# Optimization experiments

Hardware: AMD Instinct MI355X
Metric: run time of the kernel (lower is better)

## Reference

```python
import jax, jax.numpy as jnp
import numpy as np

B, T, I, H, O = 2048, 512, 1, 64, 1


def setup_inputs() -> dict:
    key = jax.random.key(0)
    ks = jax.random.split(key, 7)
    k = 1.0 / np.sqrt(H)  # PyTorch default uniform init bound
    u = lambda kk, sh: jax.random.uniform(kk, sh, jnp.float32, -k, k)
    return {
        "x": jax.random.normal(ks[0], (B, T, I), jnp.float32),
        "w_ih": u(ks[1], (4 * H, I)),   # gate order: i, f, g, o (PyTorch)
        "w_hh": u(ks[2], (4 * H, H)),
        "b_ih": u(ks[3], (4 * H,)),
        "b_hh": u(ks[4], (4 * H,)),
        "w_lin": u(ks[5], (O, H)),
        "b_lin": u(ks[6], (O,)),
    }


def _lstm_last_h(x, w_ih, w_hh, b_ih, b_hh):
    """Single-layer LSTM (PyTorch gate order i,f,g,o), returns h at the last step."""
    Bsz = x.shape[0]
    Hs = w_hh.shape[1]
    # Precompute input contribution for all timesteps: [B, T, 4H]
    gx_all = jnp.einsum('bti,gi->btg', x, w_ih) + b_ih + b_hh

    def step(carry, gx):
        h, c = carry
        g = gx + h @ w_hh.T  # [B, 4H]
        i, f, gg, o = jnp.split(g, 4, axis=-1)
        i = jax.nn.sigmoid(i)
        f = jax.nn.sigmoid(f)
        gg = jnp.tanh(gg)
        o = jax.nn.sigmoid(o)
        c = f * c + i * gg
        h = o * jnp.tanh(c)
        return (h, c), None

    h0 = jnp.zeros((Bsz, Hs), x.dtype)
    (h_last, _), _ = jax.lax.scan(step, (h0, h0), jnp.swapaxes(gx_all, 0, 1))
    return h_last  # == out[:, -1, :]


def reference(x, w_ih, w_hh, b_ih, b_hh, w_lin, b_lin):
    h = _lstm_last_h(x, w_ih, w_hh, b_ih, b_hh)
    return h @ w_lin.T + b_lin  # [B, O]
```

## Files before the change

kernel.cpp:

```cpp
#include <hip/hip_runtime.h>


typedef float    f32x4 __attribute__((ext_vector_type(4)));
typedef _Float16 f16x8 __attribute__((ext_vector_type(8)));

namespace {
constexpr int Bsz = 2048;
constexpr int Tsz = 512;
constexpr int NBW = 2;
}

__device__ __forceinline__ float rcp_f(float v)  { return __builtin_amdgcn_rcpf(v); }
__device__ __forceinline__ float exp2_f(float v) { return __builtin_amdgcn_exp2f(v); }

__device__ __forceinline__ float sigm_s(float gs)  { return rcp_f(1.0f + exp2_f(gs)); }
__device__ __forceinline__ float tanh_s(float gs)  { return fmaf(2.0f, rcp_f(1.0f + exp2_f(gs)), -1.0f); }
__device__ __forceinline__ float tanh_plain(float v) {
    return fmaf(2.0f, rcp_f(1.0f + exp2_f(v * -2.88539008178f)), -1.0f);
}

__global__ __launch_bounds__(256, 4)
void lstm_v7(const float* __restrict__ x,
             const float* __restrict__ w_ih,
             const float* __restrict__ w_hh,
             const float* __restrict__ b_ih,
             const float* __restrict__ b_hh,
             const float* __restrict__ w_lin,
             const float* __restrict__ b_lin,
             float* __restrict__ out)
{
    __shared__ __align__(16) float x_lds[Tsz][NBW];
    __shared__ __align__(16) char  hA[16 * 128];
    __shared__ __align__(16) float g_raw[256 * NBW];
    __shared__ float part[2 * NBW];

    const int tid = threadIdx.x;
    const int wv  = tid >> 6;
    const int ln  = tid & 63;
    const int col = ln & 15;
    const int grp = ln >> 4;
    const int b0  = blockIdx.x * NBW;

    constexpr float LOG2E = 1.44269504089f;
    const float s = (wv == 2) ? (-2.0f * LOG2E) : (-LOG2E);

    {
        const int b  = tid >> 7;
        const int t4 = tid & 127;
        const float4 v = ((const float4*)(x + (size_t)(b0 + b) * Tsz))[t4];
        x_lds[t4 * 4 + 0][b] = v.x;
        x_lds[t4 * 4 + 1][b] = v.y;
        x_lds[t4 * 4 + 2][b] = v.z;
        x_lds[t4 * 4 + 3][b] = v.w;
    }

    f16x8 Wf[4][2];
    float wihc[4], biasc[4];
    #pragma unroll
    for (int tn = 0; tn < 4; ++tn) {
        const int gate = wv * 64 + tn * 16 + col;
        const float* wrow = w_hh + (size_t)gate * 64;
        #pragma unroll
        for (int kc = 0; kc < 2; ++kc) {
            f16x8 w;
            #pragma unroll
            for (int e = 0; e < 8; ++e)
                w[e] = (_Float16)(wrow[kc * 32 + grp * 8 + e] * s);
            Wf[tn][kc] = w;
        }
        wihc[tn]  = w_ih[gate] * s;
        biasc[tn] = (b_ih[gate] + b_hh[gate]) * s;
    }

    const int sw    = (col & 7) << 4;
    const int aoff0 = col * 128 + ((grp * 16) ^ sw);
    const int aoff1 = col * 128 + ((64 + grp * 16) ^ sw);

    const int pb = tid & 1;
    const int pj = (tid >> 1) & 63;
    const float wlin  = w_lin[pj];
    const int   hwoff = pb * 128 + ((2 * pj) ^ (pb << 4));

    ((float2*)hA)[tid] = make_float2(0.0f, 0.0f);

    float c = 0.0f, h = 0.0f;

    __syncthreads();

    for (int t = 0; t < Tsz; ++t) {
        const float2 xb = *(const float2*)&x_lds[t][0];
        const f16x8 A0 = *(const f16x8*)(hA + aoff0);
        const f16x8 A1 = *(const f16x8*)(hA + aoff1);

        f32x4 acc[4];
        #pragma unroll
        for (int tn = 0; tn < 4; ++tn) {
            acc[tn][0] = fmaf(xb.x, wihc[tn], biasc[tn]);
            acc[tn][1] = fmaf(xb.y, wihc[tn], biasc[tn]);
            acc[tn][2] = biasc[tn];
            acc[tn][3] = biasc[tn];
        }
        #pragma unroll
        for (int tn = 0; tn < 4; ++tn)
            acc[tn] = __builtin_amdgcn_mfma_f32_16x16x32_f16(A0, Wf[tn][0], acc[tn], 0, 0, 0);
        #pragma unroll
        for (int tn = 0; tn < 4; ++tn)
            acc[tn] = __builtin_amdgcn_mfma_f32_16x16x32_f16(A1, Wf[tn][1], acc[tn], 0, 0, 0);

        if (ln < 16) {
            #pragma unroll
            for (int tn = 0; tn < 4; ++tn) {
                float2 gw;
                gw.x = acc[tn][0];
                gw.y = acc[tn][1];
                *(float2*)&g_raw[(wv * 64 + tn * 16 + ln) * 2] = gw;
            }
        }
        __syncthreads();

        if (tid < 128) {
            const float gi = g_raw[tid +   0];
            const float gf = g_raw[tid + 128];
            const float gg = g_raw[tid + 256];
            const float go = g_raw[tid + 384];

            const float ig = sigm_s(gi);
            const float fg = sigm_s(gf);
            const float tg = tanh_s(gg);
            const float og = sigm_s(go);
            c = fmaf(fg, c, ig * tg);
            h = og * tanh_plain(c);

            *(_Float16*)(hA + hwoff) = (_Float16)h;
        }
        __syncthreads();
    }

    if (tid < 128) {
        float p = h * wlin;
        #pragma unroll
        for (int off = 2; off < 64; off <<= 1)
            p += __shfl_xor(p, off, 64);
        if (ln < 2) part[wv * 2 + ln] = p;
    }
    __syncthreads();
    if (tid < NBW)
        out[b0 + tid] = part[tid] + part[2 + tid] + b_lin[0];
}

extern "C" void kernel_launch(void* const* d_in, const int* in_sizes, int n_in,
                              void* d_out, int out_size, void* d_ws, size_t ws_size,
                              hipStream_t stream) {
    const float* x     = (const float*)d_in[0];
    const float* w_ih  = (const float*)d_in[1];
    const float* w_hh  = (const float*)d_in[2];
    const float* b_ih  = (const float*)d_in[3];
    const float* b_hh  = (const float*)d_in[4];
    const float* w_lin = (const float*)d_in[5];
    const float* b_lin = (const float*)d_in[6];
    float* out = (float*)d_out;

    dim3 grid(Bsz / NBW);
    dim3 block(256);
    lstm_v7<<<grid, block, 0, stream>>>(x, w_ih, w_hh, b_ih, b_hh,
                                        w_lin, b_lin, out);
}
```

Baseline: 347.4 us.

## Ping-pong two batch chains per block to overlap MFMA with activations

```diff
diff --git a/kernel.cpp b/kernel.cpp
--- a/kernel.cpp
+++ b/kernel.cpp
@@ -7,7 +7,7 @@
 namespace {
 constexpr int Bsz = 2048;
 constexpr int Tsz = 512;
-constexpr int NBW = 2;
+constexpr int NBW = 8;
 }
 
 __device__ __forceinline__ float rcp_f(float v)  { return __builtin_amdgcn_rcpf(v); }
@@ -19,8 +19,8 @@
     return fmaf(2.0f, rcp_f(1.0f + exp2_f(v * -2.88539008178f)), -1.0f);
 }
 
-__global__ __launch_bounds__(256, 4)
-void lstm_v7(const float* __restrict__ x,
+__global__ __launch_bounds__(512, 2)
+void lstm_v8(const float* __restrict__ x,
              const float* __restrict__ w_ih,
              const float* __restrict__ w_hh,
              const float* __restrict__ b_ih,
@@ -30,9 +30,9 @@
              float* __restrict__ out)
 {
     __shared__ __align__(16) float x_lds[Tsz][NBW];
-    __shared__ __align__(16) char  hA[16 * 128];
-    __shared__ __align__(16) float g_raw[256 * NBW];
-    __shared__ float part[2 * NBW];
+    __shared__ __align__(16) char  hA[2][16 * 128];
+    __shared__ __align__(16) float g_raw[2][256 * 4];
+    __shared__ float part[32];
 
     const int tid = threadIdx.x;
     const int wv  = tid >> 6;
@@ -42,11 +42,14 @@
     const int b0  = blockIdx.x * NBW;
 
     constexpr float LOG2E = 1.44269504089f;
-    const float s = (wv == 2) ? (-2.0f * LOG2E) : (-LOG2E);
+    const int   gtype = wv >> 1;
+    const float s     = (gtype == 2) ? (-2.0f * LOG2E) : (-LOG2E);
 
-    {
-        const int b  = tid >> 7;
-        const int t4 = tid & 127;
+    #pragma unroll
+    for (int it = 0; it < 2; ++it) {
+        const int i  = tid + it * 512;
+        const int b  = i >> 7;
+        const int t4 = i & 127;
         const float4 v = ((const float4*)(x + (size_t)(b0 + b) * Tsz))[t4];
         x_lds[t4 * 4 + 0][b] = v.x;
         x_lds[t4 * 4 + 1][b] = v.y;
@@ -54,11 +57,11 @@
         x_lds[t4 * 4 + 3][b] = v.w;
     }
 
-    f16x8 Wf[4][2];
-    float wihc[4], biasc[4];
+    f16x8 Wf[2][2];
+    float wihc[2], biasc[2];
     #pragma unroll
-    for (int tn = 0; tn < 4; ++tn) {
-        const int gate = wv * 64 + tn * 16 + col;
+    for (int tn = 0; tn < 2; ++tn) {
+        const int gate = wv * 32 + tn * 16 + col;
         const float* wrow = w_hh + (size_t)gate * 64;
         #pragma unroll
         for (int kc = 0; kc < 2; ++kc) {
@@ -76,8 +79,10 @@
     const int aoff0 = col * 128 + ((grp * 16) ^ sw);
     const int aoff1 = col * 128 + ((64 + grp * 16) ^ sw);
 
-    const int pb = tid & 1;
-    const int pj = (tid >> 1) & 63;
+    const int myChain = (wv >= 4) ? 0 : 1;
+    const int idx = tid & 255;
+    const int pb  = idx & 3;
+    const int pj  = idx >> 2;
     const float wlin  = w_lin[pj];
     const int   hwoff = pb * 128 + ((2 * pj) ^ (pb << 4));
 
@@ -85,67 +90,76 @@
 
     float c = 0.0f, h = 0.0f;
 
+#define MFMA_STEP(ch, tt)                                                      \
+    {                                                                          \
+        const float4 xb = *(const float4*)&x_lds[(tt)][(ch) * 4];              \
+        const f16x8 A0 = *(const f16x8*)(hA[(ch)] + aoff0);                    \
+        const f16x8 A1 = *(const f16x8*)(hA[(ch)] + aoff1);                    \
+        f32x4 a0, a1;                                                          \
+        a0[0] = fmaf(xb.x, wihc[0], biasc[0]);                                 \
+        a0[1] = fmaf(xb.y, wihc[0], biasc[0]);                                 \
+        a0[2] = fmaf(xb.z, wihc[0], biasc[0]);                                 \
+        a0[3] = fmaf(xb.w, wihc[0], biasc[0]);                                 \
+        a1[0] = fmaf(xb.x, wihc[1], biasc[1]);                                 \
+        a1[1] = fmaf(xb.y, wihc[1], biasc[1]);                                 \
+        a1[2] = fmaf(xb.z, wihc[1], biasc[1]);                                 \
+        a1[3] = fmaf(xb.w, wihc[1], biasc[1]);                                 \
+        a0 = __builtin_amdgcn_mfma_f32_16x16x32_f16(A0, Wf[0][0], a0, 0, 0, 0);\
+        a0 = __builtin_amdgcn_mfma_f32_16x16x32_f16(A1, Wf[0][1], a0, 0, 0, 0);\
+        a1 = __builtin_amdgcn_mfma_f32_16x16x32_f16(A0, Wf[1][0], a1, 0, 0, 0);\
+        a1 = __builtin_amdgcn_mfma_f32_16x16x32_f16(A1, Wf[1][1], a1, 0, 0, 0);\
+        if (ln < 16) {                                                         \
+            *(f32x4*)&g_raw[(ch)][(wv * 32 + ln) * 4]      = a0;               \
+            *(f32x4*)&g_raw[(ch)][(wv * 32 + 16 + ln) * 4] = a1;               \
+        }                                                                      \
+    }
+
+#define ACT_STEP(ch)                                                           \
+    if (myChain == (ch)) {                                                     \
+        const float gi = g_raw[(ch)][idx +   0];                               \
+        const float gf = g_raw[(ch)][idx + 256];                               \
+        const float gg = g_raw[(ch)][idx + 512];                               \
+        const float go = g_raw[(ch)][idx + 768];                               \
+        const float ig = sigm_s(gi);                                           \
+        const float fg = sigm_s(gf);                                           \
+        const float tg = tanh_s(gg);                                           \
+        const float og = sigm_s(go);                                           \
+        c = fmaf(fg, c, ig * tg);                                              \
+        h = og * tanh_plain(c);                                                \
+        *(_Float16*)(hA[(ch)] + hwoff) = (_Float16)h;                          \
+    }
+
     __syncthreads();
 
-    for (int t = 0; t < Tsz; ++t) {
-        const float2 xb = *(const float2*)&x_lds[t][0];
-        const f16x8 A0 = *(const f16x8*)(hA + aoff0);
-        const f16x8 A1 = *(const f16x8*)(hA + aoff1);
+    MFMA_STEP(0, 0)
+    __syncthreads();
 
-        f32x4 acc[4];
-        #pragma unroll
-        for (int tn = 0; tn < 4; ++tn) {
-            acc[tn][0] = fmaf(xb.x, wihc[tn], biasc[tn]);
-            acc[tn][1] = fmaf(xb.y, wihc[tn], biasc[tn]);
-            acc[tn][2] = biasc[tn];
-            acc[tn][3] = biasc[tn];
-        }
-        #pragma unroll
-        for (int tn = 0; tn < 4; ++tn)
-            acc[tn] = __builtin_amdgcn_mfma_f32_16x16x32_f16(A0, Wf[tn][0], acc[tn], 0, 0, 0);
-        #pragma unroll
-        for (int tn = 0; tn < 4; ++tn)
-            acc[tn] = __builtin_amdgcn_mfma_f32_16x16x32_f16(A1, Wf[tn][1], acc[tn], 0, 0, 0);
-
-        if (ln < 16) {
-            #pragma unroll
-            for (int tn = 0; tn < 4; ++tn) {
-                float2 gw;
-                gw.x = acc[tn][0];
-                gw.y = acc[tn][1];
-                *(float2*)&g_raw[(wv * 64 + tn * 16 + ln) * 2] = gw;
-            }
-        }
+    for (int k = 0; k < Tsz; ++k) {
+        MFMA_STEP(1, k)
+        ACT_STEP(0)
         __syncthreads();
-
-        if (tid < 128) {
-            const float gi = g_raw[tid +   0];
-            const float gf = g_raw[tid + 128];
-            const float gg = g_raw[tid + 256];
-            const float go = g_raw[tid + 384];
-
-            const float ig = sigm_s(gi);
-            const float fg = sigm_s(gf);
-            const float tg = tanh_s(gg);
-            const float og = sigm_s(go);
-            c = fmaf(fg, c, ig * tg);
-            h = og * tanh_plain(c);
-
-            *(_Float16*)(hA + hwoff) = (_Float16)h;
-        }
+        const int kn = (k + 1) & (Tsz - 1);
+        MFMA_STEP(0, kn)
+        ACT_STEP(1)
         __syncthreads();
     }
 
-    if (tid < 128) {
-        float p = h * wlin;
-        #pragma unroll
-        for (int off = 2; off < 64; off <<= 1)
-            p += __shfl_xor(p, off, 64);
-        if (ln < 2) part[wv * 2 + ln] = p;
+#undef MFMA_STEP
+#undef ACT_STEP
+
+    float p = h * wlin;
+    #pragma unroll
+    for (int off = 4; off < 64; off <<= 1)
+        p += __shfl_xor(p, off, 64);
+    if (ln < 4) part[wv * 4 + ln] = p;
+    __syncthreads();
+    if (tid < NBW) {
+        const int wbase = (tid < 4) ? 4 : 0;
+        out[b0 + tid] = part[(wbase + 0) * 4 + (tid & 3)] +
+                        part[(wbase + 1) * 4 + (tid & 3)] +
+                        part[(wbase + 2) * 4 + (tid & 3)] +
+                        part[(wbase + 3) * 4 + (tid & 3)] + b_lin[0];
     }
-    __syncthreads();
-    if (tid < NBW)
-        out[b0 + tid] = part[tid] + part[2 + tid] + b_lin[0];
 }
 
 extern "C" void kernel_launch(void* const* d_in, const int* in_sizes, int n_in,
@@ -161,7 +175,7 @@
     float* out = (float*)d_out;
 
     dim3 grid(Bsz / NBW);
-    dim3 block(256);
-    lstm_v7<<<grid, block, 0, stream>>>(x, w_ih, w_hh, b_ih, b_hh,
+    dim3 block(512);
+    lstm_v8<<<grid, block, 0, stream>>>(x, w_ih, w_hh, b_ih, b_hh,
                                         w_lin, b_lin, out);
 }
```

New measurement: 423.4 us. +21.9%, slower.
